# Kernel optimization log

Hardware: AMD Instinct MI355X
Metric: run time of the kernel (lower is better)

## Reference

```python
import jax, jax.numpy as jnp
import numpy as np

LN_EPS = 1e-5


def setup_inputs() -> dict:
    key = jax.random.key(0)
    ks = jax.random.split(key, 5)
    B, I, H = 16384, 512, 512
    x = jax.random.normal(ks[0], (B, I), dtype=jnp.float32)
    h_prev = jax.random.normal(ks[1], (B, H), dtype=jnp.float32)
    c_prev = jax.random.normal(ks[2], (B, H), dtype=jnp.float32)
    # torch nn.Linear weight layout: [out_features, in_features]
    W = jax.random.normal(ks[3], (4 * H, I + H), dtype=jnp.float32) * (1.0 / np.sqrt(I + H))
    b = jnp.zeros((4 * H,), dtype=jnp.float32)
    gamma = jnp.ones((H,), dtype=jnp.float32)
    beta = jnp.zeros((H,), dtype=jnp.float32)
    Wp = jax.random.normal(ks[4], (H, H), dtype=jnp.float32) * (1.0 / np.sqrt(H))
    return {"x": x, "h_prev": h_prev, "c_prev": c_prev, "W": W, "b": b,
            "gamma": gamma, "beta": beta, "Wp": Wp}


def _layernorm(c, gamma, beta):
    mu = jnp.mean(c, axis=-1, keepdims=True)
    var = jnp.mean(jnp.square(c - mu), axis=-1, keepdims=True)
    return (c - mu) * jax.lax.rsqrt(var + LN_EPS) * gamma + beta


def reference(x, h_prev, c_prev, W, b, gamma, beta, Wp):
    # combined: [B, I+H]; gates: [B, 4H]
    combined = jnp.concatenate([x, h_prev], axis=1)
    gates = combined @ W.T + b
    i, f, g, o = jnp.split(gates, 4, axis=1)
    i = jax.nn.sigmoid(i)
    f = jax.nn.sigmoid(f)
    g = jnp.tanh(g)
    o = jax.nn.sigmoid(o)
    cell = f * c_prev + i * g
    cell = _layernorm(cell, gamma, beta)
    out = (o * jnp.tanh(cell)) @ Wp.T  # projection, no bias
    return (out, cell)
```

## Files before the change

kernel.cpp:

```cpp
#include <hip/hip_runtime.h>
#include <hip/hip_bf16.h>


typedef __attribute__((ext_vector_type(4))) float f32x4;
typedef __attribute__((ext_vector_type(8))) short bf16x8;
typedef __attribute__((ext_vector_type(4))) short bf16x4;

#define NB 16384
#define NH 512

__device__ __forceinline__ short f2bf(float f) {
    union { float f; unsigned u; } v; v.f = f;
    unsigned r = v.u + 0x7FFFu + ((v.u >> 16) & 1u);
    return (short)(r >> 16);
}
__device__ __forceinline__ float bf2f(short s) {
    union { unsigned u; float f; } v; v.u = ((unsigned)(unsigned short)s) << 16;
    return v.f;
}
__device__ __forceinline__ float sigmoidf_(float x) { return 1.0f / (1.0f + __expf(-x)); }
__device__ __forceinline__ float tanhf_(float x) { return 1.0f - 2.0f / (__expf(2.0f * x) + 1.0f); }

__device__ __forceinline__ void gld16(const void* g, void* l) {
    __builtin_amdgcn_global_load_lds(
        (const __attribute__((address_space(1))) void*)g,
        (__attribute__((address_space(3))) void*)l, 16, 0, 0);
}

__global__ __launch_bounds__(256)
void k_convert_A(const float* __restrict__ x, const float* __restrict__ h,
                 short* __restrict__ Abf)
{
    const long long total = (long long)NB * 256;
    long long i = (long long)blockIdx.x * 256 + threadIdx.x;
    const long long stride = (long long)gridDim.x * 256;
    for (; i < total; i += stride) {
        const int r  = (int)(i >> 8);
        const int c4 = (int)(i & 255);
        const float* src = (c4 < 128) ? (x + (size_t)r * 512 + c4 * 4)
                                      : (h + (size_t)r * 512 + (c4 - 128) * 4);
        f32x4 v = *(const f32x4*)src;
        bf16x4 o;
#pragma unroll
        for (int j = 0; j < 4; ++j) o[j] = f2bf(v[j]);
        *(bf16x4*)(Abf + i * 4) = o;
    }
}

__global__ __launch_bounds__(256)
void k_convert_W(const float* __restrict__ W, const float* __restrict__ Wp,
                 short* __restrict__ Wbf, short* __restrict__ Wpbf)
{
    const long long nW  = (long long)2048 * 1024 / 4;
    const long long nWp = (long long)512 * 512 / 4;
    long long i = (long long)blockIdx.x * 256 + threadIdx.x;
    const long long stride = (long long)gridDim.x * 256;
    for (; i < nW + nWp; i += stride) {
        f32x4 v; short* dst;
        if (i < nW) { v = *(const f32x4*)(W + i * 4); dst = Wbf + i * 4; }
        else { v = *(const f32x4*)(Wp + (i - nW) * 4); dst = Wpbf + (i - nW) * 4; }
        bf16x4 o;
#pragma unroll
        for (int j = 0; j < 4; ++j) o[j] = f2bf(v[j]);
        *(bf16x4*)dst = o;
    }
}

__global__ __launch_bounds__(256, 3)
void k_gates_cell(const short* __restrict__ Abf, const short* __restrict__ Wbf,
                  const float* __restrict__ c_prev, const float* __restrict__ bvec,
                  float* __restrict__ cell_raw, short* __restrict__ o_ws)
{
    __shared__ __align__(16) short As[128 * 64];
    __shared__ __align__(16) short Bs[128 * 64];

    const int tid  = threadIdx.x;
    const int lane = tid & 63;
    const int wid  = tid >> 6;
    const int wr = wid >> 1, wc = wid & 1;
    const int row0 = blockIdx.x * 128;
    const int h0   = blockIdx.y * 32;

    const f32x4 zero = {0.f, 0.f, 0.f, 0.f};
    f32x4 acc[4][4];
#pragma unroll
    for (int m = 0; m < 4; ++m)
#pragma unroll
        for (int n = 0; n < 4; ++n) acc[m][n] = zero;

    const int k8 = ((lane & 7) ^ (lane >> 3)) * 8;
    int aOff[4], bOff[4];
#pragma unroll
    for (int j = 0; j < 4; ++j) {
        const int row = (wid * 4 + j) * 8 + (lane >> 3);
        aOff[j] = (row0 + row) * 1024 + k8;
        const int gate = (row >> 4) & 3;
        const int wrow = gate * 512 + h0 + (row >> 6) * 16 + (row & 15);
        bOff[j] = wrow * 1024 + k8;
    }

    for (int kt = 0; kt < 16; ++kt) {
        const int kbase = kt * 64;
#pragma unroll
        for (int j = 0; j < 4; ++j) {
            gld16(Abf + aOff[j] + kbase, As + (wid * 4 + j) * 512);
            gld16(Wbf + bOff[j] + kbase, Bs + (wid * 4 + j) * 512);
        }
        __syncthreads();
#pragma unroll
        for (int kk = 0; kk < 64; kk += 32) {
            bf16x8 af[4], bfr[4];
#pragma unroll
            for (int m = 0; m < 4; ++m) {
                const int row = wr * 64 + m * 16 + (lane & 15);
                int byt = row * 128 + (kk + (lane >> 4) * 8) * 2;
                byt ^= (row & 7) << 4;
                af[m] = *(const bf16x8*)((const char*)As + byt);
            }
#pragma unroll
            for (int n = 0; n < 4; ++n) {
                const int row = wc * 64 + n * 16 + (lane & 15);
                int byt = row * 128 + (kk + (lane >> 4) * 8) * 2;
                byt ^= (row & 7) << 4;
                bfr[n] = *(const bf16x8*)((const char*)Bs + byt);
            }
#pragma unroll
            for (int m = 0; m < 4; ++m)
#pragma unroll
                for (int n = 0; n < 4; ++n)
                    acc[m][n] = __builtin_amdgcn_mfma_f32_16x16x32_bf16(af[m], bfr[n], acc[m][n], 0, 0, 0);
        }
        __syncthreads();
    }

    const int hcol = h0 + wc * 16 + (lane & 15);
    float bias[4];
#pragma unroll
    for (int n = 0; n < 4; ++n) bias[n] = bvec[n * 512 + hcol];
#pragma unroll
    for (int m = 0; m < 4; ++m) {
        const int rbase = row0 + wr * 64 + m * 16 + ((lane >> 4) * 4);
#pragma unroll
        for (int q = 0; q < 4; ++q) {
            const size_t idx = (size_t)(rbase + q) * 512 + hcol;
            const float iv = acc[m][0][q] + bias[0];
            const float fv = acc[m][1][q] + bias[1];
            const float gv = acc[m][2][q] + bias[2];
            const float ov = acc[m][3][q] + bias[3];
            const float c = c_prev[idx];
            cell_raw[idx] = sigmoidf_(fv) * c + sigmoidf_(iv) * tanhf_(gv);
            o_ws[idx] = f2bf(sigmoidf_(ov));
        }
    }
}

__global__ __launch_bounds__(256)
void k_layernorm(const float* __restrict__ gamma, const float* __restrict__ beta,
                 float* __restrict__ cell, short* __restrict__ s_io)
{
    const int r = blockIdx.x * 4 + (threadIdx.x >> 6);
    const int lane = threadIdx.x & 63;
    float* row = cell + (size_t)r * 512;
    f32x4 v0 = *(const f32x4*)(row + lane * 8);
    f32x4 v1 = *(const f32x4*)(row + lane * 8 + 4);
    float s1 = 0.f, s2 = 0.f;
#pragma unroll
    for (int j = 0; j < 4; ++j) {
        s1 += v0[j] + v1[j];
        s2 += v0[j] * v0[j] + v1[j] * v1[j];
    }
#pragma unroll
    for (int off = 32; off > 0; off >>= 1) {
        s1 += __shfl_xor(s1, off);
        s2 += __shfl_xor(s2, off);
    }
    const float mu  = s1 * (1.f / 512.f);
    const float var = s2 * (1.f / 512.f) - mu * mu;
    const float rs  = rsqrtf(var + 1e-5f);
    const f32x4 g0 = *(const f32x4*)(gamma + lane * 8);
    const f32x4 g1 = *(const f32x4*)(gamma + lane * 8 + 4);
    const f32x4 b0 = *(const f32x4*)(beta + lane * 8);
    const f32x4 b1 = *(const f32x4*)(beta + lane * 8 + 4);
    const bf16x8 o8 = *(const bf16x8*)(s_io + (size_t)r * 512 + lane * 8);
    f32x4 c0, c1; bf16x8 s8;
#pragma unroll
    for (int j = 0; j < 4; ++j) {
        c0[j] = (v0[j] - mu) * rs * g0[j] + b0[j];
        c1[j] = (v1[j] - mu) * rs * g1[j] + b1[j];
    }
#pragma unroll
    for (int j = 0; j < 4; ++j) {
        s8[j]     = f2bf(bf2f(o8[j])     * tanhf_(c0[j]));
        s8[j + 4] = f2bf(bf2f(o8[j + 4]) * tanhf_(c1[j]));
    }
    *(f32x4*)(row + lane * 8)     = c0;
    *(f32x4*)(row + lane * 8 + 4) = c1;
    *(bf16x8*)(s_io + (size_t)r * 512 + lane * 8) = s8;
}

__global__ __launch_bounds__(256, 3)
void k_proj(const short* __restrict__ s_ws, const short* __restrict__ Wpbf,
            float* __restrict__ out)
{
    __shared__ __align__(16) short As[128 * 64];
    __shared__ __align__(16) short Bs[128 * 64];
    const int tid = threadIdx.x;
    const int lane = tid & 63;
    const int wid = tid >> 6;
    const int wr = wid >> 1, wc = wid & 1;
    const int row0 = blockIdx.x * 128;
    const int col0 = blockIdx.y * 128;

    const f32x4 zero = {0.f, 0.f, 0.f, 0.f};
    f32x4 acc[4][4];
#pragma unroll
    for (int m = 0; m < 4; ++m)
#pragma unroll
        for (int n = 0; n < 4; ++n) acc[m][n] = zero;

    const int k8 = ((lane & 7) ^ (lane >> 3)) * 8;
    int aOff[4], bOff[4];
#pragma unroll
    for (int j = 0; j < 4; ++j) {
        const int row = (wid * 4 + j) * 8 + (lane >> 3);
        aOff[j] = (row0 + row) * 512 + k8;
        bOff[j] = (col0 + row) * 512 + k8;
    }

    for (int kt = 0; kt < 8; ++kt) {
        const int kbase = kt * 64;
#pragma unroll
        for (int j = 0; j < 4; ++j) {
            gld16(s_ws + aOff[j] + kbase, As + (wid * 4 + j) * 512);
            gld16(Wpbf + bOff[j] + kbase, Bs + (wid * 4 + j) * 512);
        }
        __syncthreads();
#pragma unroll
        for (int kk = 0; kk < 64; kk += 32) {
            bf16x8 af[4], bfr[4];
#pragma unroll
            for (int m = 0; m < 4; ++m) {
                const int row = wr * 64 + m * 16 + (lane & 15);
                int byt = row * 128 + (kk + (lane >> 4) * 8) * 2;
                byt ^= (row & 7) << 4;
                af[m] = *(const bf16x8*)((const char*)As + byt);
            }
#pragma unroll
            for (int n = 0; n < 4; ++n) {
                const int row = wc * 64 + n * 16 + (lane & 15);
                int byt = row * 128 + (kk + (lane >> 4) * 8) * 2;
                byt ^= (row & 7) << 4;
                bfr[n] = *(const bf16x8*)((const char*)Bs + byt);
            }
#pragma unroll
            for (int m = 0; m < 4; ++m)
#pragma unroll
                for (int n = 0; n < 4; ++n)
                    acc[m][n] = __builtin_amdgcn_mfma_f32_16x16x32_bf16(af[m], bfr[n], acc[m][n], 0, 0, 0);
        }
        __syncthreads();
    }

#pragma unroll
    for (int m = 0; m < 4; ++m) {
        const int grow = row0 + wr * 64 + m * 16 + ((lane >> 4) * 4);
#pragma unroll
        for (int n = 0; n < 4; ++n) {
            const int gcol = col0 + wc * 64 + n * 16 + (lane & 15);
#pragma unroll
            for (int q = 0; q < 4; ++q)
                out[(size_t)(grow + q) * 512 + gcol] = acc[m][n][q];
        }
    }
}

extern "C" void kernel_launch(void* const* d_in, const int* in_sizes, int n_in,
                              void* d_out, int out_size, void* d_ws, size_t ws_size,
                              hipStream_t stream) {
    (void)in_sizes; (void)n_in; (void)out_size; (void)ws_size;
    const float* x      = (const float*)d_in[0];
    const float* h_prev = (const float*)d_in[1];
    const float* c_prev = (const float*)d_in[2];
    const float* W      = (const float*)d_in[3];
    const float* bvec   = (const float*)d_in[4];
    const float* gamma  = (const float*)d_in[5];
    const float* beta   = (const float*)d_in[6];
    const float* Wp     = (const float*)d_in[7];

    float* out  = (float*)d_out;
    float* cell = out + (size_t)NB * NH;
    short* Abf  = (short*)d_out;
    short* s_io = (short*)d_ws;
    short* Wbf  = s_io + (size_t)NB * NH;
    short* Wpbf = Wbf + (size_t)2048 * 1024;

    k_convert_A<<<2048, 256, 0, stream>>>(x, h_prev, Abf);
    k_convert_W<<<1024, 256, 0, stream>>>(W, Wp, Wbf, Wpbf);
    dim3 g1(NB / 128, 2048 / 128);
    k_gates_cell<<<g1, 256, 0, stream>>>(Abf, Wbf, c_prev, bvec, cell, s_io);
    k_layernorm<<<NB / 4, 256, 0, stream>>>(gamma, beta, cell, s_io);
    dim3 g3(NB / 128, NH / 128);
    k_proj<<<g3, 256, 0, stream>>>(s_io, Wpbf, out);
}
```

Before: 264.6 us.

## Double-buffer LDS tiles in both GEMMs and merge convert kernels

```diff
diff --git a/kernel.cpp b/kernel.cpp
--- a/kernel.cpp
+++ b/kernel.cpp
@@ -28,37 +28,32 @@
 }
 
 __global__ __launch_bounds__(256)
-void k_convert_A(const float* __restrict__ x, const float* __restrict__ h,
-                 short* __restrict__ Abf)
+void k_convert(const float* __restrict__ x, const float* __restrict__ h,
+               const float* __restrict__ W, const float* __restrict__ Wp,
+               short* __restrict__ Abf, short* __restrict__ Wbf,
+               short* __restrict__ Wpbf)
 {
-    const long long total = (long long)NB * 256;
-    long long i = (long long)blockIdx.x * 256 + threadIdx.x;
-    const long long stride = (long long)gridDim.x * 256;
-    for (; i < total; i += stride) {
-        const int r  = (int)(i >> 8);
-        const int c4 = (int)(i & 255);
-        const float* src = (c4 < 128) ? (x + (size_t)r * 512 + c4 * 4)
-                                      : (h + (size_t)r * 512 + (c4 - 128) * 4);
-        f32x4 v = *(const f32x4*)src;
-        bf16x4 o;
-#pragma unroll
-        for (int j = 0; j < 4; ++j) o[j] = f2bf(v[j]);
-        *(bf16x4*)(Abf + i * 4) = o;
-    }
-}
-
-__global__ __launch_bounds__(256)
-void k_convert_W(const float* __restrict__ W, const float* __restrict__ Wp,
-                 short* __restrict__ Wbf, short* __restrict__ Wpbf)
-{
+    const long long nA  = (long long)NB * 256;
     const long long nW  = (long long)2048 * 1024 / 4;
     const long long nWp = (long long)512 * 512 / 4;
     long long i = (long long)blockIdx.x * 256 + threadIdx.x;
     const long long stride = (long long)gridDim.x * 256;
-    for (; i < nW + nWp; i += stride) {
-        f32x4 v; short* dst;
-        if (i < nW) { v = *(const f32x4*)(W + i * 4); dst = Wbf + i * 4; }
-        else { v = *(const f32x4*)(Wp + (i - nW) * 4); dst = Wpbf + (i - nW) * 4; }
+    for (; i < nA + nW + nWp; i += stride) {
+        const float* src; short* dst;
+        if (i < nA) {
+            const int r  = (int)(i >> 8);
+            const int c4 = (int)(i & 255);
+            src = (c4 < 128) ? (x + (size_t)r * 512 + c4 * 4)
+                             : (h + (size_t)r * 512 + (c4 - 128) * 4);
+            dst = Abf + i * 4;
+        } else if (i < nA + nW) {
+            const long long j = i - nA;
+            src = W + j * 4; dst = Wbf + j * 4;
+        } else {
+            const long long j = i - nA - nW;
+            src = Wp + j * 4; dst = Wpbf + j * 4;
+        }
+        f32x4 v = *(const f32x4*)src;
         bf16x4 o;
 #pragma unroll
         for (int j = 0; j < 4; ++j) o[j] = f2bf(v[j]);
@@ -66,13 +61,13 @@
     }
 }
 
-__global__ __launch_bounds__(256, 3)
+__global__ __launch_bounds__(256, 2)
 void k_gates_cell(const short* __restrict__ Abf, const short* __restrict__ Wbf,
                   const float* __restrict__ c_prev, const float* __restrict__ bvec,
                   float* __restrict__ cell_raw, short* __restrict__ o_ws)
 {
-    __shared__ __align__(16) short As[128 * 64];
-    __shared__ __align__(16) short Bs[128 * 64];
+    __shared__ __align__(16) short As[2][128 * 64];
+    __shared__ __align__(16) short Bs[2][128 * 64];
 
     const int tid  = threadIdx.x;
     const int lane = tid & 63;
@@ -89,6 +84,7 @@
         for (int n = 0; n < 4; ++n) acc[m][n] = zero;
 
     const int k8 = ((lane & 7) ^ (lane >> 3)) * 8;
+    const int ldsc = (wid * 4) * 512;
     int aOff[4], bOff[4];
 #pragma unroll
     for (int j = 0; j < 4; ++j) {
@@ -99,14 +95,25 @@
         bOff[j] = wrow * 1024 + k8;
     }
 
+#pragma unroll
+    for (int j = 0; j < 4; ++j) {
+        gld16(Abf + aOff[j], &As[0][ldsc + j * 512]);
+        gld16(Wbf + bOff[j], &Bs[0][ldsc + j * 512]);
+    }
+    __syncthreads();
+
+    int cur = 0;
     for (int kt = 0; kt < 16; ++kt) {
-        const int kbase = kt * 64;
-#pragma unroll
-        for (int j = 0; j < 4; ++j) {
-            gld16(Abf + aOff[j] + kbase, As + (wid * 4 + j) * 512);
-            gld16(Wbf + bOff[j] + kbase, Bs + (wid * 4 + j) * 512);
-        }
-        __syncthreads();
+        if (kt < 15) {
+            const int kb = (kt + 1) * 64;
+#pragma unroll
+            for (int j = 0; j < 4; ++j) {
+                gld16(Abf + aOff[j] + kb, &As[cur ^ 1][ldsc + j * 512]);
+                gld16(Wbf + bOff[j] + kb, &Bs[cur ^ 1][ldsc + j * 512]);
+            }
+        }
+        const short* Ac = As[cur];
+        const short* Bc = Bs[cur];
 #pragma unroll
         for (int kk = 0; kk < 64; kk += 32) {
             bf16x8 af[4], bfr[4];
@@ -115,14 +122,14 @@
                 const int row = wr * 64 + m * 16 + (lane & 15);
                 int byt = row * 128 + (kk + (lane >> 4) * 8) * 2;
                 byt ^= (row & 7) << 4;
-                af[m] = *(const bf16x8*)((const char*)As + byt);
+                af[m] = *(const bf16x8*)((const char*)Ac + byt);
             }
 #pragma unroll
             for (int n = 0; n < 4; ++n) {
                 const int row = wc * 64 + n * 16 + (lane & 15);
                 int byt = row * 128 + (kk + (lane >> 4) * 8) * 2;
                 byt ^= (row & 7) << 4;
-                bfr[n] = *(const bf16x8*)((const char*)Bs + byt);
+                bfr[n] = *(const bf16x8*)((const char*)Bc + byt);
             }
 #pragma unroll
             for (int m = 0; m < 4; ++m)
@@ -131,6 +138,7 @@
                     acc[m][n] = __builtin_amdgcn_mfma_f32_16x16x32_bf16(af[m], bfr[n], acc[m][n], 0, 0, 0);
         }
         __syncthreads();
+        cur ^= 1;
     }
 
     const int hcol = h0 + wc * 16 + (lane & 15);
@@ -198,12 +206,12 @@
     *(bf16x8*)(s_io + (size_t)r * 512 + lane * 8) = s8;
 }
 
-__global__ __launch_bounds__(256, 3)
+__global__ __launch_bounds__(256, 2)
 void k_proj(const short* __restrict__ s_ws, const short* __restrict__ Wpbf,
             float* __restrict__ out)
 {
-    __shared__ __align__(16) short As[128 * 64];
-    __shared__ __align__(16) short Bs[128 * 64];
+    __shared__ __align__(16) short As[2][128 * 64];
+    __shared__ __align__(16) short Bs[2][128 * 64];
     const int tid = threadIdx.x;
     const int lane = tid & 63;
     const int wid = tid >> 6;
@@ -219,6 +227,7 @@
         for (int n = 0; n < 4; ++n) acc[m][n] = zero;
 
     const int k8 = ((lane & 7) ^ (lane >> 3)) * 8;
+    const int ldsc = (wid * 4) * 512;
     int aOff[4], bOff[4];
 #pragma unroll
     for (int j = 0; j < 4; ++j) {
@@ -227,14 +236,25 @@
         bOff[j] = (col0 + row) * 512 + k8;
     }
 
+#pragma unroll
+    for (int j = 0; j < 4; ++j) {
+        gld16(s_ws + aOff[j], &As[0][ldsc + j * 512]);
+        gld16(Wpbf + bOff[j], &Bs[0][ldsc + j * 512]);
+    }
+    __syncthreads();
+
+    int cur = 0;
     for (int kt = 0; kt < 8; ++kt) {
-        const int kbase = kt * 64;
-#pragma unroll
-        for (int j = 0; j < 4; ++j) {
-            gld16(s_ws + aOff[j] + kbase, As + (wid * 4 + j) * 512);
-            gld16(Wpbf + bOff[j] + kbase, Bs + (wid * 4 + j) * 512);
-        }
-        __syncthreads();
+        if (kt < 7) {
+            const int kb = (kt + 1) * 64;
+#pragma unroll
+            for (int j = 0; j < 4; ++j) {
+                gld16(s_ws + aOff[j] + kb, &As[cur ^ 1][ldsc + j * 512]);
+                gld16(Wpbf + bOff[j] + kb, &Bs[cur ^ 1][ldsc + j * 512]);
+            }
+        }
+        const short* Ac = As[cur];
+        const short* Bc = Bs[cur];
 #pragma unroll
         for (int kk = 0; kk < 64; kk += 32) {
             bf16x8 af[4], bfr[4];
@@ -243,14 +263,14 @@
                 const int row = wr * 64 + m * 16 + (lane & 15);
                 int byt = row * 128 + (kk + (lane >> 4) * 8) * 2;
                 byt ^= (row & 7) << 4;
-                af[m] = *(const bf16x8*)((const char*)As + byt);
+                af[m] = *(const bf16x8*)((const char*)Ac + byt);
             }
 #pragma unroll
             for (int n = 0; n < 4; ++n) {
                 const int row = wc * 64 + n * 16 + (lane & 15);
                 int byt = row * 128 + (kk + (lane >> 4) * 8) * 2;
                 byt ^= (row & 7) << 4;
-                bfr[n] = *(const bf16x8*)((const char*)Bs + byt);
+                bfr[n] = *(const bf16x8*)((const char*)Bc + byt);
             }
 #pragma unroll
             for (int m = 0; m < 4; ++m)
@@ -259,6 +279,7 @@
                     acc[m][n] = __builtin_amdgcn_mfma_f32_16x16x32_bf16(af[m], bfr[n], acc[m][n], 0, 0, 0);
         }
         __syncthreads();
+        cur ^= 1;
     }
 
 #pragma unroll
@@ -294,8 +315,7 @@
     short* Wbf  = s_io + (size_t)NB * NH;
     short* Wpbf = Wbf + (size_t)2048 * 1024;
 
-    k_convert_A<<<2048, 256, 0, stream>>>(x, h_prev, Abf);
-    k_convert_W<<<1024, 256, 0, stream>>>(W, Wp, Wbf, Wpbf);
+    k_convert<<<2048, 256, 0, stream>>>(x, h_prev, W, Wp, Abf, Wbf, Wpbf);
     dim3 g1(NB / 128, 2048 / 128);
     k_gates_cell<<<g1, 256, 0, stream>>>(Abf, Wbf, c_prev, bvec, cell, s_io);
     k_layernorm<<<NB / 4, 256, 0, stream>>>(gamma, beta, cell, s_io);
```

Result: slower. 272.2 us (+2.9%).
